# Kernel tuning notes

Hardware: AMD Instinct MI355X
Metric: run time of the kernel (lower is better)

Reference implementation:

```python
import jax, jax.numpy as jnp
import numpy as np

B, T, D = 4, 2048, 1024
H = 16
DK = D // H
SCALE = 1.0 / np.sqrt(DK)
EPS_LN = 1e-5
EPS_NORM = 1e-8


def setup_inputs() -> dict:
    key = jax.random.key(0)
    ks = jax.random.split(key, 12)
    gain = 1.0 / np.sqrt(2.0)
    # xavier_uniform bound for square [D, D] weight with gain
    bound = gain * np.sqrt(6.0 / (D + D))

    def w(k):
        return jax.random.uniform(k, (D, D), jnp.float32, -bound, bound)

    return {
        "x": jax.random.normal(ks[0], (B, T, D), jnp.float32),
        "mask": jax.random.bernoulli(ks[1], 0.1, (B, T)),  # True = masked out
        "wq": w(ks[2]), "bq": jnp.zeros((D,), jnp.float32),
        "wk": w(ks[3]), "bk": jnp.zeros((D,), jnp.float32),
        "wv": w(ks[4]), "bv": jnp.zeros((D,), jnp.float32),
        "wo": w(ks[5]), "bo": jnp.zeros((D,), jnp.float32),
        "ln_g": jnp.ones((D,), jnp.float32),
        "ln_b": jnp.zeros((D,), jnp.float32),
    }


def _layernorm(x, g, b):
    mu = jnp.mean(x, axis=-1, keepdims=True)
    var = jnp.var(x, axis=-1, keepdims=True)
    return (x - mu) * jax.lax.rsqrt(var + EPS_LN) * g + b


def _l2norm(x):
    # torch F.normalize: x / clamp_min(||x||_2, eps)
    n = jnp.sqrt(jnp.sum(x * x, axis=-1, keepdims=True))
    return x / jnp.maximum(n, EPS_NORM)


def reference(x, mask, wq, bq, wk, bk, wv, bv, wo, bo, ln_g, ln_b):
    xn = _layernorm(x, ln_g, ln_b)  # q_norm applied to shared input

    def proj(w, bias):
        y = jnp.einsum("btd,ed->bte", xn, w) + bias
        return y.reshape(B, T, H, DK).transpose(0, 2, 1, 3)  # [B,H,T,DK]

    Q = _l2norm(proj(wq, bq))
    K = _l2norm(proj(wk, bk))
    V = proj(wv, bv)

    scores = jnp.einsum("bhqd,bhkd->bhqk", Q, K) * SCALE
    scores = jnp.clip(scores, -10.0, 10.0)
    scores = jnp.where(mask[:, None, None, :], -10000.0, scores)
    scores = scores - jnp.max(scores, axis=-1, keepdims=True)
    attn = jax.nn.softmax(scores, axis=-1)

    out = jnp.einsum("bhqk,bhkd->bhqd", attn, V)
    out = out.transpose(0, 2, 1, 3).reshape(B, T, D)
    out = jnp.einsum("btd,ed->bte", out, wo) + bo
    return out * 0.5
```

## Files before the change

### kernel.cpp

```cpp
#include <hip/hip_runtime.h>
#include <hip/hip_bf16.h>
#include <cstdint>
#include <cstddef>
#include <cstring>

typedef unsigned short u16;
typedef unsigned char u8;
typedef __attribute__((ext_vector_type(8))) short short8;
typedef __attribute__((ext_vector_type(4))) float f32x4;

#define B_    4
#define T_    2048
#define D_    1024
#define H_    16
#define DK_   64
#define QSCALE_ 0.18033688011112042f

__device__ __forceinline__ float bf2f(u16 u) {
    unsigned int x = ((unsigned int)u) << 16;
    float f; __builtin_memcpy(&f, &x, 4); return f;
}
__device__ __forceinline__ u16 f2bf(float f) {
    unsigned int x; __builtin_memcpy(&x, &f, 4);
    x += 0x7fffu + ((x >> 16) & 1u);
    return (u16)(x >> 16);
}

__global__ __launch_bounds__(256) void prep_kernel(
    const u16* __restrict__ x, const u8* __restrict__ m,
    const void* s0, const void* s1, const void* s2, const void* s3,
    const void* s4, const void* s5,
    u16* __restrict__ vecs, u8* __restrict__ nm, int* flag, int n)
{
    __shared__ int tot, sbits;
    int tid = threadIdx.x;
    if (tid == 0) { tot = 0; sbits = 0; }
    __syncthreads();
    int cnt = 0;
    for (int i = tid; i < 4096; i += 256) {
        int e = (x[2 * i] >> 7) & 0xFF;
        if (e > 137 || (e >= 1 && e < 97)) cnt++;
    }
    int bits = 0;
    for (int i = tid; i < n; i += 256)
        if (m[i]) bits |= (i & 7);
    for (int o = 1; o < 64; o <<= 1) { cnt += __shfl_xor(cnt, o); bits |= __shfl_xor(bits, o); }
    if ((tid & 63) == 0) { atomicAdd(&tot, cnt); if (bits) atomicOr(&sbits, bits); }
    __syncthreads();
    int f = (tot > 1024) ? 1 : 0;
    if (tid == 0) *flag = f;
    int b = sbits;
    int stride = (b & 1) ? 1 : (b & 2) ? 2 : (b & 4) ? 4 : 8;
    for (int i = tid; i < n; i += 256)
        nm[i] = m[(size_t)i * stride] ? 1 : 0;
    const void* ss[6] = {s0, s1, s2, s3, s4, s5};
    for (int t = 0; t < 6; t++) {
        const void* s = ss[t];
        for (int i = tid; i < 1024; i += 256)
            vecs[t * 1024 + i] = f ? f2bf(((const float*)s)[i]) : ((const u16*)s)[i];
    }
}

__global__ __launch_bounds__(256) void convert_w_kernel(
    const void* s0, const void* s1, const void* s2, const void* s3,
    u16* d0, u16* d1, u16* d2, u16* d3, const int* __restrict__ flag)
{
    const void* s; u16* d;
    if (blockIdx.y == 0)      { s = s0; d = d0; }
    else if (blockIdx.y == 1) { s = s1; d = d1; }
    else if (blockIdx.y == 2) { s = s2; d = d2; }
    else                      { s = s3; d = d3; }
    int i4 = blockIdx.x * 256 + threadIdx.x;
    if (*flag) {
        float4 v = ((const float4*)s)[i4];
        ushort4 o; o.x = f2bf(v.x); o.y = f2bf(v.y); o.z = f2bf(v.z); o.w = f2bf(v.w);
        ((ushort4*)d)[i4] = o;
    } else {
        ((ushort4*)d)[i4] = ((const ushort4*)s)[i4];
    }
}

__global__ __launch_bounds__(256) void ln_kernel(
    const void* __restrict__ x, const u16* __restrict__ g,
    const u16* __restrict__ be, u16* __restrict__ xn, const int* __restrict__ flag)
{
    int row = blockIdx.x;
    int t = threadIdx.x;
    float v[4];
    if (*flag) {
        float4 f4 = ((const float4*)x)[(size_t)row * 256 + t];
        v[0] = f4.x; v[1] = f4.y; v[2] = f4.z; v[3] = f4.w;
    } else {
        ushort4 uv = ((const ushort4*)x)[(size_t)row * 256 + t];
        v[0] = bf2f(uv.x); v[1] = bf2f(uv.y); v[2] = bf2f(uv.z); v[3] = bf2f(uv.w);
    }
    float s = v[0] + v[1] + v[2] + v[3];
    float q = v[0]*v[0] + v[1]*v[1] + v[2]*v[2] + v[3]*v[3];
    for (int o = 1; o < 64; o <<= 1) { s += __shfl_xor(s, o); q += __shfl_xor(q, o); }
    __shared__ float rs[4], rq[4];
    int wv = t >> 6, ln = t & 63;
    if (ln == 0) { rs[wv] = s; rq[wv] = q; }
    __syncthreads();
    s = rs[0] + rs[1] + rs[2] + rs[3];
    q = rq[0] + rq[1] + rq[2] + rq[3];
    float mu   = s * (1.0f / D_);
    float var  = q * (1.0f / D_) - mu * mu;
    float rstd = rsqrtf(var + 1e-5f);
    u16 o4[4];
    for (int i = 0; i < 4; i++) {
        float f = (v[i] - mu) * rstd * bf2f(g[t*4 + i]) + bf2f(be[t*4 + i]);
        o4[i] = f2bf(f);
    }
    ushort4 ov; ov.x = o4[0]; ov.y = o4[1]; ov.z = o4[2]; ov.w = o4[3];
    *(ushort4*)(xn + (size_t)row * D_ + t * 4) = ov;
}

__global__ __launch_bounds__(256) void gemm_bt(
    const u16* __restrict__ A,
    const u16* __restrict__ W0, const u16* __restrict__ W1, const u16* __restrict__ W2,
    const u16* __restrict__ bias_all, int bias_idx0,
    u16* __restrict__ C0, u16* __restrict__ C1, u16* __restrict__ C2,
    float scale, const int* __restrict__ flag, int use_flag, int qkv_mode)
{
    const int K = 1024, N = 1024;
    const u16* W; const u16* bias; u16* C;
    if (blockIdx.z == 0)      { W = W0; bias = bias_all + (size_t)bias_idx0 * 1024;       C = C0; }
    else if (blockIdx.z == 1) { W = W1; bias = bias_all + (size_t)(bias_idx0 + 1) * 1024; C = C1; }
    else                      { W = W2; bias = bias_all + (size_t)(bias_idx0 + 2) * 1024; C = C2; }

    __shared__ u16 As[128 * 32];
    __shared__ u16 Bs[128 * 32];

    int tid  = threadIdx.x;
    int wave = tid >> 6, lane = tid & 63;
    int wm = wave >> 1, wn = wave & 1;
    int quad = lane >> 4, l16 = lane & 15;
    int bm = blockIdx.y * 128, bn = blockIdx.x * 128;

    f32x4 acc[4][4];
    const f32x4 fz = {0.f, 0.f, 0.f, 0.f};
    for (int i = 0; i < 4; i++) for (int j = 0; j < 4; j++) acc[i][j] = fz;

    int srow = lane >> 2;
    int scol = (lane & 3) * 8;
    const u16* gA0 = A + (size_t)(bm + wave * 32 + srow) * K + scol;
    const u16* gB0 = W + (size_t)(bn + wave * 32 + srow) * K + scol;

    for (int k0 = 0; k0 < K; k0 += 32) {
        for (int i = 0; i < 2; i++) {
            __builtin_amdgcn_global_load_lds(
                (const __attribute__((address_space(1))) void*)(gA0 + (size_t)i * 16 * K + k0),
                (__attribute__((address_space(3))) void*)(As + (wave * 32 + i * 16) * 32),
                16, 0, 0);
            __builtin_amdgcn_global_load_lds(
                (const __attribute__((address_space(1))) void*)(gB0 + (size_t)i * 16 * K + k0),
                (__attribute__((address_space(3))) void*)(Bs + (wave * 32 + i * 16) * 32),
                16, 0, 0);
        }
        __syncthreads();
        short8 a[4], b[4];
        for (int i = 0; i < 4; i++)
            a[i] = *(const short8*)(As + (wm * 64 + i * 16 + l16) * 32 + quad * 8);
        for (int j = 0; j < 4; j++)
            b[j] = *(const short8*)(Bs + (wn * 64 + j * 16 + l16) * 32 + quad * 8);
        for (int i = 0; i < 4; i++)
            for (int j = 0; j < 4; j++)
                acc[i][j] = __builtin_amdgcn_mfma_f32_16x16x32_bf16(a[i], b[j], acc[i][j], 0, 0, 0);
        __syncthreads();
    }

    if (qkv_mode) {
        if (blockIdx.z == 2) {
            for (int j = 0; j < 4; j++) {
                int col = bn + wn * 64 + j * 16 + l16;
                int h = col >> 6, d = col & 63;
                float bi = bf2f(bias[col]);
                for (int i = 0; i < 4; i++) {
                    int row0 = bm + wm * 64 + i * 16 + quad * 4;
                    int bq = row0 >> 11, t0 = row0 & 2047;
                    ushort4 pk;
                    pk.x = f2bf(acc[i][j][0] + bi); pk.y = f2bf(acc[i][j][1] + bi);
                    pk.z = f2bf(acc[i][j][2] + bi); pk.w = f2bf(acc[i][j][3] + bi);
                    *(ushort4*)(C + ((size_t)((bq * 16 + h) * 64 + d)) * 2048 + t0) = pk;
                }
            }
        } else {
            float sc2 = (blockIdx.z == 0) ? QSCALE_ : 1.0f;
            float bi[4];
            for (int j = 0; j < 4; j++) bi[j] = bf2f(bias[bn + wn * 64 + j * 16 + l16]);
            for (int i = 0; i < 4; i++) {
                int row0 = bm + wm * 64 + i * 16 + quad * 4;
                for (int r = 0; r < 4; r++) {
                    float v[4]; float s = 0.f;
                    for (int j = 0; j < 4; j++) { v[j] = acc[i][j][r] + bi[j]; s += v[j] * v[j]; }
                    s += __shfl_xor(s, 1); s += __shfl_xor(s, 2);
                    s += __shfl_xor(s, 4); s += __shfl_xor(s, 8);
                    float scl = sc2 / fmaxf(sqrtf(s), 1e-8f);
                    for (int j = 0; j < 4; j++) {
                        int col = bn + wn * 64 + j * 16 + l16;
                        C[(size_t)(row0 + r) * N + col] = f2bf(v[j] * scl);
                    }
                }
            }
        }
        return;
    }

    int f32out = use_flag ? *flag : 0;
    for (int j = 0; j < 4; j++) {
        int col = bn + wn * 64 + j * 16 + l16;
        float bi = bf2f(bias[col]);
        for (int i = 0; i < 4; i++) {
            int row0 = bm + wm * 64 + i * 16 + quad * 4;
            for (int r = 0; r < 4; r++) {
                float o = (acc[i][j][r] + bi) * scale;
                if (f32out) ((float*)C)[(size_t)(row0 + r) * N + col] = o;
                else        C[(size_t)(row0 + r) * N + col] = f2bf(o);
            }
        }
    }
}

__global__ __launch_bounds__(256, 3) void attn_kernel(
    const u16* __restrict__ Q, const u16* __restrict__ Kg,
    const u16* __restrict__ Vt, const u8* __restrict__ nm,
    u16* __restrict__ Oout)
{
    __shared__ u16 Ks[64 * 72];
    __shared__ u16 VTs[64 * 72];
    __shared__ u16 Ps[128 * 72];
    __shared__ __align__(16) float msf[64];
    __shared__ float l_sh[128];

    int tid  = threadIdx.x;
    int wave = tid >> 6, lane = tid & 63;
    int quad = lane >> 4, l16 = lane & 15;
    int L  = blockIdx.x + (blockIdx.y << 4);
    int bh = (L & 7) + ((L >> 7) << 3);
    int q0 = ((L >> 3) & 15) * 128;
    int b  = bh >> 4, h = bh & 15;
    const size_t base  = (size_t)b * T_ * D_ + h * DK_;
    const size_t vbase = (size_t)((b * 16 + h) * 64) * T_;

    short8 qa[2][2];
    for (int g = 0; g < 2; g++) {
        const u16* qrow = Q + base + (size_t)(q0 + wave * 32 + g * 16 + l16) * D_;
        qa[g][0] = *(const short8*)(qrow + quad * 8);
        qa[g][1] = *(const short8*)(qrow + 32 + quad * 8);
    }

    int sr = tid >> 3;
    int sc = (tid & 7) * 8;
    const u8* mrow = nm + b * T_;

    for (int p = 0; p < 2; p++) {
        int r = sr + p * 32;
        *(short8*)(&Ks[r * 72 + sc])  = *(const short8*)(Kg + base + (size_t)r * D_ + sc);
        *(short8*)(&VTs[r * 72 + sc]) = *(const short8*)(Vt + vbase + (size_t)r * T_ + sc);
    }
    if (tid < 64) msf[tid] = mrow[tid] ? 0.f : 1.f;
    __syncthreads();

    const f32x4 fz = {0.f, 0.f, 0.f, 0.f};
    f32x4 o_acc[2][4];
    for (int g = 0; g < 2; g++) for (int j = 0; j < 4; j++) o_acc[g][j] = fz;
    float rowsum[2] = {0.f, 0.f};

    for (int kt = 0; kt < T_; kt += 64) {
        int ktn = (kt + 64) & (T_ - 1);
        short8 kpre[2], vpre[2];
        for (int p = 0; p < 2; p++) {
            int r = sr + p * 32;
            kpre[p] = *(const short8*)(Kg + base + (size_t)(ktn + r) * D_ + sc);
            vpre[p] = *(const short8*)(Vt + vbase + (size_t)r * T_ + ktn + sc);
        }
        u8 mpre = (tid < 64) ? mrow[ktn + tid] : (u8)0;

        for (int j = 0; j < 4; j++) {
            short8 kb0 = *(const short8*)(Ks + (j * 16 + l16) * 72 + quad * 8);
            short8 kb1 = *(const short8*)(Ks + (j * 16 + l16) * 72 + 32 + quad * 8);
            f32x4 pm4 = *(const f32x4*)&msf[j * 16 + quad * 4];
            for (int g = 0; g < 2; g++) {
                f32x4 s4 = __builtin_amdgcn_mfma_f32_16x16x32_bf16(kb0, qa[g][0], fz, 0, 0, 0);
                s4       = __builtin_amdgcn_mfma_f32_16x16x32_bf16(kb1, qa[g][1], s4, 0, 0, 0);
                float p0 = __builtin_exp2f(s4[0]) * pm4[0];
                float p1 = __builtin_exp2f(s4[1]) * pm4[1];
                float p2 = __builtin_exp2f(s4[2]) * pm4[2];
                float p3 = __builtin_exp2f(s4[3]) * pm4[3];
                rowsum[g] += (p0 + p1) + (p2 + p3);
                __hip_bfloat162 h01 = __float22bfloat162_rn(float2{p0, p1});
                __hip_bfloat162 h23 = __float22bfloat162_rn(float2{p2, p3});
                uint2 pk;
                __builtin_memcpy(&pk.x, &h01, 4);
                __builtin_memcpy(&pk.y, &h23, 4);
                *(uint2*)(Ps + (wave * 32 + g * 16 + l16) * 72 + j * 16 + quad * 4) = pk;
            }
        }

        short8 pa0[2], pa1[2];
        for (int g = 0; g < 2; g++) {
            pa0[g] = *(const short8*)(Ps + (wave * 32 + g * 16 + l16) * 72 + quad * 8);
            pa1[g] = *(const short8*)(Ps + (wave * 32 + g * 16 + l16) * 72 + 32 + quad * 8);
        }
        for (int j = 0; j < 4; j++) {
            short8 vb0 = *(const short8*)(VTs + (j * 16 + l16) * 72 + quad * 8);
            short8 vb1 = *(const short8*)(VTs + (j * 16 + l16) * 72 + 32 + quad * 8);
            for (int g = 0; g < 2; g++) {
                o_acc[g][j] = __builtin_amdgcn_mfma_f32_16x16x32_bf16(pa0[g], vb0, o_acc[g][j], 0, 0, 0);
                o_acc[g][j] = __builtin_amdgcn_mfma_f32_16x16x32_bf16(pa1[g], vb1, o_acc[g][j], 0, 0, 0);
            }
        }

        __syncthreads();
        for (int p = 0; p < 2; p++) {
            int r = sr + p * 32;
            *(short8*)(&Ks[r * 72 + sc])  = kpre[p];
            *(short8*)(&VTs[r * 72 + sc]) = vpre[p];
        }
        if (tid < 64) msf[tid] = mpre ? 0.f : 1.f;
        __syncthreads();
    }

    for (int g = 0; g < 2; g++) {
        float l = rowsum[g];
        l += __shfl_xor(l, 16);
        l += __shfl_xor(l, 32);
        if (quad == 0) l_sh[wave * 32 + g * 16 + l16] = l;
    }

    for (int g = 0; g < 2; g++) {
        for (int j = 0; j < 4; j++) {
            for (int r = 0; r < 4; r++) {
                int row = wave * 32 + g * 16 + quad * 4 + r;
                float ld = fmaxf(l_sh[row], 1e-20f);
                float o = o_acc[g][j][r] / ld;
                Oout[base + (size_t)(q0 + row) * D_ + j * 16 + l16] = f2bf(o);
            }
        }
    }
}

extern "C" void kernel_launch(void* const* d_in, const int* in_sizes, int n_in,
                              void* d_out, int out_size, void* d_ws, size_t ws_size,
                              hipStream_t stream)
{
    const void* x    = d_in[0];
    const u8*   mask = (const u8*)d_in[1];
    const void* wq   = d_in[2];
    const void* bq   = d_in[3];
    const void* wk   = d_in[4];
    const void* bk   = d_in[5];
    const void* wv   = d_in[6];
    const void* bv   = d_in[7];
    const void* wo   = d_in[8];
    const void* bo   = d_in[9];
    const void* lng  = d_in[10];
    const void* lnb  = d_in[11];

    const size_t NTOK = (size_t)B_ * T_;
    u16* xn  = (u16*)d_ws;
    u16* Kb  = xn + NTOK * D_;
    u16* Vtb = Kb + NTOK * D_;
    u16* wqc = Vtb + NTOK * D_;
    u16* wkc = wqc + (size_t)D_ * D_;
    u16* wvc = wkc + (size_t)D_ * D_;
    u16* woc = wvc + (size_t)D_ * D_;
    u16* vecs = woc + (size_t)D_ * D_;
    u8*  nm  = (u8*)(vecs + 6 * 1024);
    int* flag = (int*)(nm + 8192);
    u16* Qb  = (u16*)d_out;

    prep_kernel<<<dim3(1), 256, 0, stream>>>((const u16*)x, mask, bq, bk, bv, bo, lng, lnb,
                                             vecs, nm, flag, B_ * T_);
    convert_w_kernel<<<dim3(1024, 4), 256, 0, stream>>>(wq, wk, wv, wo, wqc, wkc, wvc, woc, flag);
    ln_kernel<<<dim3(NTOK), 256, 0, stream>>>(x, vecs + 4 * 1024, vecs + 5 * 1024, xn, flag);
    gemm_bt<<<dim3(8, 64, 3), 256, 0, stream>>>(xn, wqc, wkc, wvc, vecs, 0, Qb, Kb, Vtb, 1.0f, flag, 0, 1);
    attn_kernel<<<dim3(16, 64), 256, 0, stream>>>(Qb, Kb, Vtb, nm, xn);
    gemm_bt<<<dim3(8, 64, 1), 256, 0, stream>>>(xn, woc, woc, woc, vecs, 3, (u16*)d_out, (u16*)d_out, (u16*)d_out, 0.5f, flag, 1, 0);
}
```

Before: 384.4 us.

## Load K/V MFMA fragments directly from global memory, drop LDS staging and barriers

The attention kernel no longer stages K and V tiles in shared memory with register prefetch and two block barriers per iteration. Each wave now reads its MFMA operand fragments straight from global memory and relies on L1/L2 caching across the four waves that share them. The mask becomes an additive float bias in the exponent instead of a multiplicative 0/1 factor, and occupancy is raised to 4 blocks per SM. This removes LDS traffic and synchronisation, but exposes global-load latency with no explicit prefetch and adds redundant global reads across waves.

```diff
diff --git a/kernel.cpp b/kernel.cpp
--- a/kernel.cpp
+++ b/kernel.cpp
@@ -30,7 +30,7 @@
     const u16* __restrict__ x, const u8* __restrict__ m,
     const void* s0, const void* s1, const void* s2, const void* s3,
     const void* s4, const void* s5,
-    u16* __restrict__ vecs, u8* __restrict__ nm, int* flag, int n)
+    u16* __restrict__ vecs, float* __restrict__ mbias, int* flag, int n)
 {
     __shared__ int tot, sbits;
     int tid = threadIdx.x;
@@ -52,7 +52,7 @@
     int b = sbits;
     int stride = (b & 1) ? 1 : (b & 2) ? 2 : (b & 4) ? 4 : 8;
     for (int i = tid; i < n; i += 256)
-        nm[i] = m[(size_t)i * stride] ? 1 : 0;
+        mbias[i] = m[(size_t)i * stride] ? -30000.f : 0.f;
     const void* ss[6] = {s0, s1, s2, s3, s4, s5};
     for (int t = 0; t < 6; t++) {
         const void* s = ss[t];
@@ -221,15 +221,12 @@
     }
 }
 
-__global__ __launch_bounds__(256, 3) void attn_kernel(
+__global__ __launch_bounds__(256, 4) void attn_kernel(
     const u16* __restrict__ Q, const u16* __restrict__ Kg,
-    const u16* __restrict__ Vt, const u8* __restrict__ nm,
+    const u16* __restrict__ Vt, const float* __restrict__ mbias,
     u16* __restrict__ Oout)
 {
-    __shared__ u16 Ks[64 * 72];
-    __shared__ u16 VTs[64 * 72];
     __shared__ u16 Ps[128 * 72];
-    __shared__ __align__(16) float msf[64];
     __shared__ float l_sh[128];
 
     int tid  = threadIdx.x;
@@ -249,76 +246,53 @@
         qa[g][1] = *(const short8*)(qrow + 32 + quad * 8);
     }
 
-    int sr = tid >> 3;
-    int sc = (tid & 7) * 8;
-    const u8* mrow = nm + b * T_;
-
-    for (int p = 0; p < 2; p++) {
-        int r = sr + p * 32;
-        *(short8*)(&Ks[r * 72 + sc])  = *(const short8*)(Kg + base + (size_t)r * D_ + sc);
-        *(short8*)(&VTs[r * 72 + sc]) = *(const short8*)(Vt + vbase + (size_t)r * T_ + sc);
-    }
-    if (tid < 64) msf[tid] = mrow[tid] ? 0.f : 1.f;
-    __syncthreads();
+    const float* mrow = mbias + b * T_;
+    const u16* kfrag = Kg + base + (size_t)l16 * D_ + quad * 8;
+    const u16* vfrag = Vt + vbase + (size_t)l16 * T_ + quad * 8;
 
     const f32x4 fz = {0.f, 0.f, 0.f, 0.f};
     f32x4 o_acc[2][4];
     for (int g = 0; g < 2; g++) for (int j = 0; j < 4; j++) o_acc[g][j] = fz;
     float rowsum[2] = {0.f, 0.f};
 
+    u16* psw = Ps + (wave * 32 + l16) * 72;
+    const u16* psr = Ps + (wave * 32 + l16) * 72;
+
     for (int kt = 0; kt < T_; kt += 64) {
-        int ktn = (kt + 64) & (T_ - 1);
-        short8 kpre[2], vpre[2];
-        for (int p = 0; p < 2; p++) {
-            int r = sr + p * 32;
-            kpre[p] = *(const short8*)(Kg + base + (size_t)(ktn + r) * D_ + sc);
-            vpre[p] = *(const short8*)(Vt + vbase + (size_t)r * T_ + ktn + sc);
-        }
-        u8 mpre = (tid < 64) ? mrow[ktn + tid] : (u8)0;
-
         for (int j = 0; j < 4; j++) {
-            short8 kb0 = *(const short8*)(Ks + (j * 16 + l16) * 72 + quad * 8);
-            short8 kb1 = *(const short8*)(Ks + (j * 16 + l16) * 72 + 32 + quad * 8);
-            f32x4 pm4 = *(const f32x4*)&msf[j * 16 + quad * 4];
+            short8 kb0 = *(const short8*)(kfrag + (size_t)(kt + j * 16) * D_);
+            short8 kb1 = *(const short8*)(kfrag + (size_t)(kt + j * 16) * D_ + 32);
+            float4 mb4 = *(const float4*)(mrow + kt + j * 16 + quad * 4);
             for (int g = 0; g < 2; g++) {
                 f32x4 s4 = __builtin_amdgcn_mfma_f32_16x16x32_bf16(kb0, qa[g][0], fz, 0, 0, 0);
                 s4       = __builtin_amdgcn_mfma_f32_16x16x32_bf16(kb1, qa[g][1], s4, 0, 0, 0);
-                float p0 = __builtin_exp2f(s4[0]) * pm4[0];
-                float p1 = __builtin_exp2f(s4[1]) * pm4[1];
-                float p2 = __builtin_exp2f(s4[2]) * pm4[2];
-                float p3 = __builtin_exp2f(s4[3]) * pm4[3];
+                float p0 = __builtin_exp2f(s4[0] + mb4.x);
+                float p1 = __builtin_exp2f(s4[1] + mb4.y);
+                float p2 = __builtin_exp2f(s4[2] + mb4.z);
+                float p3 = __builtin_exp2f(s4[3] + mb4.w);
                 rowsum[g] += (p0 + p1) + (p2 + p3);
                 __hip_bfloat162 h01 = __float22bfloat162_rn(float2{p0, p1});
                 __hip_bfloat162 h23 = __float22bfloat162_rn(float2{p2, p3});
                 uint2 pk;
                 __builtin_memcpy(&pk.x, &h01, 4);
                 __builtin_memcpy(&pk.y, &h23, 4);
-                *(uint2*)(Ps + (wave * 32 + g * 16 + l16) * 72 + j * 16 + quad * 4) = pk;
+                *(uint2*)(psw + g * 16 * 72 + j * 16 + quad * 4) = pk;
             }
         }
 
         short8 pa0[2], pa1[2];
         for (int g = 0; g < 2; g++) {
-            pa0[g] = *(const short8*)(Ps + (wave * 32 + g * 16 + l16) * 72 + quad * 8);
-            pa1[g] = *(const short8*)(Ps + (wave * 32 + g * 16 + l16) * 72 + 32 + quad * 8);
+            pa0[g] = *(const short8*)(psr + g * 16 * 72 + quad * 8);
+            pa1[g] = *(const short8*)(psr + g * 16 * 72 + 32 + quad * 8);
         }
         for (int j = 0; j < 4; j++) {
-            short8 vb0 = *(const short8*)(VTs + (j * 16 + l16) * 72 + quad * 8);
-            short8 vb1 = *(const short8*)(VTs + (j * 16 + l16) * 72 + 32 + quad * 8);
+            short8 vb0 = *(const short8*)(vfrag + (size_t)(j * 16) * T_ + kt);
+            short8 vb1 = *(const short8*)(vfrag + (size_t)(j * 16) * T_ + kt + 32);
             for (int g = 0; g < 2; g++) {
                 o_acc[g][j] = __builtin_amdgcn_mfma_f32_16x16x32_bf16(pa0[g], vb0, o_acc[g][j], 0, 0, 0);
                 o_acc[g][j] = __builtin_amdgcn_mfma_f32_16x16x32_bf16(pa1[g], vb1, o_acc[g][j], 0, 0, 0);
             }
         }
-
-        __syncthreads();
-        for (int p = 0; p < 2; p++) {
-            int r = sr + p * 32;
-            *(short8*)(&Ks[r * 72 + sc])  = kpre[p];
-            *(short8*)(&VTs[r * 72 + sc]) = vpre[p];
-        }
-        if (tid < 64) msf[tid] = mpre ? 0.f : 1.f;
-        __syncthreads();
     }
 
     for (int g = 0; g < 2; g++) {
@@ -366,15 +340,15 @@
     u16* wvc = wkc + (size_t)D_ * D_;
     u16* woc = wvc + (size_t)D_ * D_;
     u16* vecs = woc + (size_t)D_ * D_;
-    u8*  nm  = (u8*)(vecs + 6 * 1024);
-    int* flag = (int*)(nm + 8192);
+    float* mbias = (float*)(vecs + 6 * 1024);
+    int* flag = (int*)(mbias + 8192);
     u16* Qb  = (u16*)d_out;
 
     prep_kernel<<<dim3(1), 256, 0, stream>>>((const u16*)x, mask, bq, bk, bv, bo, lng, lnb,
-                                             vecs, nm, flag, B_ * T_);
+                                             vecs, mbias, flag, B_ * T_);
     convert_w_kernel<<<dim3(1024, 4), 256, 0, stream>>>(wq, wk, wv, wo, wqc, wkc, wvc, woc, flag);
     ln_kernel<<<dim3(NTOK), 256, 0, stream>>>(x, vecs + 4 * 1024, vecs + 5 * 1024, xn, flag);
     gemm_bt<<<dim3(8, 64, 3), 256, 0, stream>>>(xn, wqc, wkc, wvc, vecs, 0, Qb, Kb, Vtb, 1.0f, flag, 0, 1);
-    attn_kernel<<<dim3(16, 64), 256, 0, stream>>>(Qb, Kb, Vtb, nm, xn);
+    attn_kernel<<<dim3(16, 64), 256, 0, stream>>>(Qb, Kb, Vtb, mbias, xn);
     gemm_bt<<<dim3(8, 64, 1), 256, 0, stream>>>(xn, woc, woc, woc, vecs, 3, (u16*)d_out, (u16*)d_out, (u16*)d_out, 0.5f, flag, 1, 0);
 }
```

Result: slower. 499.3 us (+29.9%).
